# Optimization experiments

Measured on AMD Instinct MI355X. Metric: run time of the kernel, lower is better.

The kernel has to match this reference:

```python
import jax, jax.numpy as jnp
import numpy as np

D = 256       # d_model
NH = 8        # heads
K = 7         # neighborhood kernel size
DFF = 1024    # feedforward dim
EPS = 1e-5
B, H, W = 4, 56, 56


def layer_norm(x, g, b):
    m = jnp.mean(x, axis=-1, keepdims=True)
    v = jnp.mean((x - m) ** 2, axis=-1, keepdims=True)
    return (x - m) * jax.lax.rsqrt(v + EPS) * g + b


def neighborhood_attn(x, W_qkv, b_qkv, W_proj, b_proj):
    # NATTEN NeighborhoodAttention2D: each query attends to a KxK window
    # centered on it, clamped (shifted) at borders so every query sees K*K keys.
    Bx, Hx, Wx, C = x.shape
    hd = C // NH
    qkv = x @ W_qkv + b_qkv                      # [B,H,W,3C]
    q, k, v = jnp.split(qkv, 3, axis=-1)
    q = q.reshape(Bx, Hx, Wx, NH, hd)
    k = k.reshape(Bx, Hx, Wx, NH, hd)
    v = v.reshape(Bx, Hx, Wx, NH, hd)
    # neighbor index grids: start = clip(i - K//2, 0, H-K), window = start + [0..K)
    ih = jnp.clip(jnp.arange(Hx) - K // 2, 0, Hx - K)[:, None] + jnp.arange(K)  # [H,K]
    iw = jnp.clip(jnp.arange(Wx) - K // 2, 0, Wx - K)[:, None] + jnp.arange(K)  # [W,K]
    # gather K/V neighborhoods -> [B,H,W,K,K,NH,hd]
    k_nb = k[:, ih[:, None, :, None], iw[None, :, None, :]]
    v_nb = v[:, ih[:, None, :, None], iw[None, :, None, :]]
    attn = jnp.einsum('bhwnd,bhwijnd->bhwnij', q, k_nb) * (hd ** -0.5)
    attn = jax.nn.softmax(attn.reshape(Bx, Hx, Wx, NH, K * K), axis=-1)
    attn = attn.reshape(Bx, Hx, Wx, NH, K, K)
    out = jnp.einsum('bhwnij,bhwijnd->bhwnd', attn, v_nb).reshape(Bx, Hx, Wx, C)
    return out @ W_proj + b_proj


def setup_inputs() -> dict:
    key = jax.random.key(0)
    ks = jax.random.split(key, 8)
    s = 0.02
    return {
        'x': jax.random.normal(ks[0], (B, H, W, D), dtype=jnp.float32),
        'W_qkv': jax.random.normal(ks[1], (D, 3 * D), dtype=jnp.float32) * s,
        'b_qkv': jnp.zeros((3 * D,), dtype=jnp.float32),
        'W_proj': jax.random.normal(ks[2], (D, D), dtype=jnp.float32) * s,
        'b_proj': jnp.zeros((D,), dtype=jnp.float32),
        'W1': jax.random.normal(ks[3], (D, DFF), dtype=jnp.float32) * s,
        'b1': jnp.zeros((DFF,), dtype=jnp.float32),
        'W2': jax.random.normal(ks[4], (DFF, D), dtype=jnp.float32) * s,
        'b2': jnp.zeros((D,), dtype=jnp.float32),
        'g1': jnp.ones((D,), dtype=jnp.float32),
        'be1': jnp.zeros((D,), dtype=jnp.float32),
        'g2': jnp.ones((D,), dtype=jnp.float32),
        'be2': jnp.zeros((D,), dtype=jnp.float32),
    }


def reference(x, W_qkv, b_qkv, W_proj, b_proj, W1, b1, W2, b2, g1, be1, g2, be2):
    # norm_first=False (post-norm): x = norm1(x + mha(x)); x = norm2(x + ff(x))
    a = neighborhood_attn(x, W_qkv, b_qkv, W_proj, b_proj)
    x = layer_norm(x + a, g1, be1)
    f = jax.nn.relu(x @ W1 + b1) @ W2 + b2
    return layer_norm(x + f, g2, be2)
```

## Files before the change

kernel.cpp:

```cpp
#include <hip/hip_runtime.h>
#include <math.h>

#define BATCH 4
#define HH 56
#define WW 56
#define DMODEL 256
#define NHEADS 8
#define HD 32
#define NNB 49
#define NTOK (BATCH*HH*WW)

#define HALO 22
#define NHTOK (HALO*HALO)
#define KV_PAD 40

typedef __attribute__((ext_vector_type(8))) short s16x8;
typedef __attribute__((ext_vector_type(4))) float f32x4;
typedef __attribute__((ext_vector_type(2))) float f32x2;

__device__ inline unsigned short f2b(float f) {
    union { float f; unsigned int u; } v; v.f = f;
    unsigned int r = v.u + 0x7FFF + ((v.u >> 16) & 1);
    return (unsigned short)(r >> 16);
}
__device__ inline float b2f(unsigned short u) {
    union { float f; unsigned int u; } v; v.u = ((unsigned int)u) << 16;
    return v.f;
}

__device__ __forceinline__ f32x2 unpk(unsigned int u) {
    union { unsigned int u; float f; } lo, hi;
    lo.u = u << 16;
    hi.u = u & 0xffff0000u;
    return f32x2{lo.f, hi.f};
}

__device__ __forceinline__ f32x2 pk_fma(f32x2 a, f32x2 b, f32x2 c) {
#if __has_builtin(__builtin_elementwise_fma)
    return __builtin_elementwise_fma(a, b, c);
#else
    return f32x2{fmaf(a.x, b.x, c.x), fmaf(a.y, b.y, c.y)};
#endif
}

__device__ __forceinline__ void async16(const unsigned short* g, unsigned short* l) {
    __builtin_amdgcn_global_load_lds(
        (const __attribute__((address_space(1))) unsigned int*)g,
        (__attribute__((address_space(3))) unsigned int*)l, 16, 0, 0);
}

#define WAITV(N) { asm volatile("s_waitcnt vmcnt(" #N ")" ::: "memory"); }
#define BAR()    { __builtin_amdgcn_s_barrier(); __builtin_amdgcn_sched_barrier(0); }

#define XCAST_BLOCKS 1568

__device__ __forceinline__ void transpose_tile(
    const float* __restrict__ src, unsigned short* __restrict__ dst,
    int K, int N, int kt, int nt, int tid, float* lds )
{
    const int k0 = kt * 64, n0 = nt * 64;
    #pragma unroll
    for (int p = 0; p < 4; ++p) {
        const int r  = p * 16 + (tid >> 4);
        const int c4 = (tid & 15) * 4;
        const float4 v = *(const float4*)(src + (size_t)(k0 + r) * N + n0 + c4);
        lds[r * 65 + c4 + 0] = v.x; lds[r * 65 + c4 + 1] = v.y;
        lds[r * 65 + c4 + 2] = v.z; lds[r * 65 + c4 + 3] = v.w;
    }
    __syncthreads();
    #pragma unroll
    for (int p = 0; p < 4; ++p) {
        const int c  = p * 16 + (tid >> 4);
        const int k4 = (tid & 15) * 4;
        ushort4 o;
        o.x = f2b(lds[(k4 + 0) * 65 + c]);
        o.y = f2b(lds[(k4 + 1) * 65 + c]);
        o.z = f2b(lds[(k4 + 2) * 65 + c]);
        o.w = f2b(lds[(k4 + 3) * 65 + c]);
        *(ushort4*)(dst + (size_t)(n0 + c) * K + k0 + k4) = o;
    }
}

__global__ __launch_bounds__(256)
void prep_kernel(const float* __restrict__ x,
                 const float* __restrict__ Wq, const float* __restrict__ Wp,
                 const float* __restrict__ W1, const float* __restrict__ W2,
                 unsigned short* __restrict__ xb,
                 unsigned short* __restrict__ Wqb, unsigned short* __restrict__ Wpb,
                 unsigned short* __restrict__ W1b, unsigned short* __restrict__ W2b)
{
    __shared__ float lds[64 * 65];
    const int tid = threadIdx.x;
    if (blockIdx.x < XCAST_BLOCKS) {
        const int i = blockIdx.x * 256 + tid;
        const float4* xp = (const float4*)x + (size_t)i * 2;
        const float4 a = xp[0], b = xp[1];
        s16x8 o;
        o[0] = (short)f2b(a.x); o[1] = (short)f2b(a.y);
        o[2] = (short)f2b(a.z); o[3] = (short)f2b(a.w);
        o[4] = (short)f2b(b.x); o[5] = (short)f2b(b.y);
        o[6] = (short)f2b(b.z); o[7] = (short)f2b(b.w);
        *((s16x8*)xb + i) = o;
        return;
    }
    int wb = blockIdx.x - XCAST_BLOCKS;
    if (wb < 48) {
        transpose_tile(Wq, Wqb, 256, 768, wb & 3, wb >> 2, tid, lds);
    } else if ((wb -= 48) < 16) {
        transpose_tile(Wp, Wpb, 256, 256, wb & 3, wb >> 2, tid, lds);
    } else if ((wb -= 16) < 64) {
        transpose_tile(W1, W1b, 256, 1024, wb & 3, wb >> 2, tid, lds);
    } else {
        wb -= 64;
        transpose_tile(W2, W2b, 1024, 256, wb & 15, wb >> 4, tid, lds);
    }
}

__global__ __launch_bounds__(256)
void gemm_k(const unsigned short* __restrict__ Ab,
            const unsigned short* __restrict__ Bt, const float* __restrict__ bias,
            unsigned short* __restrict__ outb,
            int N, int K, int relu)
{
    __shared__ unsigned short As[2][128 * 64];
    __shared__ unsigned short Bs[2][128 * 64];

    const int tid = threadIdx.x;

    const int nwg = gridDim.x;
    const int q8 = nwg >> 3, r8 = nwg & 7;
    const int xcd = blockIdx.x & 7, pos = blockIdx.x >> 3;
    const int d = (xcd < r8 ? xcd * (q8 + 1) : r8 * (q8 + 1) + (xcd - r8) * q8) + pos;
    const int nbx = N >> 7;
    const int bm = (d / nbx) * 128, bn = (d % nbx) * 128;

    const int wid = tid >> 6, lane = tid & 63;
    const int wm = (wid >> 1) * 64, wn = (wid & 1) * 64;
    const int row16 = lane & 15, quad = lane >> 4;
    const int crow = lane >> 3;
    const int ckS = ((lane & 7) ^ crow) * 8;

    f32x4 acc[4][4] = {};

    auto stage = [&](int buf, int k0) {
        #pragma unroll
        for (int c = 0; c < 4; ++c) {
            const int ch = wid * 4 + c;
            async16(Ab + (size_t)(bm + ch * 8 + crow) * K + k0 + ckS, As[buf] + ch * 512);
        }
        #pragma unroll
        for (int c = 0; c < 4; ++c) {
            const int ch = wid * 4 + c;
            async16(Bt + (size_t)(bn + ch * 8 + crow) * K + k0 + ckS, Bs[buf] + ch * 512);
        }
    };
    auto compute = [&](int buf) {
        #pragma unroll
        for (int kc = 0; kc < 2; ++kc) {
            s16x8 af[4], bf[4];
            #pragma unroll
            for (int i = 0; i < 4; ++i)
                af[i] = *(const s16x8*)(As[buf] + (wm + i * 16 + row16) * 64
                                        + (((kc * 4 + quad) ^ (row16 & 7)) * 8));
            #pragma unroll
            for (int j = 0; j < 4; ++j)
                bf[j] = *(const s16x8*)(Bs[buf] + (wn + j * 16 + row16) * 64
                                        + (((kc * 4 + quad) ^ (row16 & 7)) * 8));
            #pragma unroll
            for (int i = 0; i < 4; ++i)
                #pragma unroll
                for (int j = 0; j < 4; ++j)
                    acc[i][j] = __builtin_amdgcn_mfma_f32_16x16x32_bf16(af[i], bf[j], acc[i][j], 0, 0, 0);
        }
    };

    stage(0, 0);
    stage(1, 64);
    const int nsteps = K >> 6;
    for (int s = 0; s < nsteps; ++s) {
        const int buf = s & 1;
        if (s == nsteps - 1) WAITV(0) else WAITV(8)
        BAR()
        compute(buf);
        BAR()
        if (s + 2 < nsteps) stage(buf, (s + 2) << 6);
    }

    unsigned short* Cs = (unsigned short*)As;
    #pragma unroll
    for (int j = 0; j < 4; ++j) {
        const int col = wn + j * 16 + row16;
        const float bb = bias[bn + col];
        #pragma unroll
        for (int i = 0; i < 4; ++i) {
            const int rr = wm + i * 16 + quad * 4;
            #pragma unroll
            for (int reg = 0; reg < 4; ++reg) {
                float v = acc[i][j][reg] + bb;
                if (relu) v = fmaxf(v, 0.f);
                Cs[(rr + reg) * 128 + col] = f2b(v);
            }
        }
    }
    __syncthreads();
    #pragma unroll
    for (int p = 0; p < 8; ++p) {
        const int s = p * 256 + tid;
        const int rr = s >> 4, cb = (s & 15) * 8;
        *(s16x8*)(outb + (size_t)(bm + rr) * N + bn + cb) = *(const s16x8*)(Cs + rr * 128 + cb);
    }
}

__global__ __launch_bounds__(512)
void gemm_ln(const unsigned short* __restrict__ Ab, const unsigned short* __restrict__ Bt,
             const float* __restrict__ bias, const float* __restrict__ resid,
             const float* __restrict__ g, const float* __restrict__ beta,
             float* __restrict__ outf, unsigned short* __restrict__ outb, int K)
{
    __shared__ unsigned short As[2][64 * 64];
    __shared__ unsigned short Bs[2][256 * 64];

    const int tid = threadIdx.x;
    const int bm = blockIdx.x * 64;
    const int wid = tid >> 6, lane = tid & 63;
    const int wm = (wid >> 2) * 32, wn = (wid & 3) * 64;
    const int wc = wid & 3;
    const int row16 = lane & 15, quad = lane >> 4;
    const int crow = lane >> 3;
    const int ckS = ((lane & 7) ^ crow) * 8;

    f32x4 acc[2][4] = {};

    auto stage = [&](int buf, int k0) {
        #pragma unroll
        for (int c = 0; c < 5; ++c) {
            const int ch = wid * 5 + c;
            if (ch < 8) {
                async16(Ab + (size_t)(bm + ch * 8 + crow) * K + k0 + ckS, As[buf] + ch * 512);
            } else {
                const int bc = ch - 8;
                async16(Bt + (size_t)(bc * 8 + crow) * K + k0 + ckS, Bs[buf] + bc * 512);
            }
        }
    };
    auto compute = [&](int buf) {
        #pragma unroll
        for (int kc = 0; kc < 2; ++kc) {
            s16x8 af[2], bf[4];
            #pragma unroll
            for (int i = 0; i < 2; ++i)
                af[i] = *(const s16x8*)(As[buf] + (wm + i * 16 + row16) * 64
                                        + (((kc * 4 + quad) ^ (row16 & 7)) * 8));
            #pragma unroll
            for (int j = 0; j < 4; ++j)
                bf[j] = *(const s16x8*)(Bs[buf] + (wn + j * 16 + row16) * 64
                                        + (((kc * 4 + quad) ^ (row16 & 7)) * 8));
            #pragma unroll
            for (int i = 0; i < 2; ++i)
                #pragma unroll
                for (int j = 0; j < 4; ++j)
                    acc[i][j] = __builtin_amdgcn_mfma_f32_16x16x32_bf16(af[i], bf[j], acc[i][j], 0, 0, 0);
        }
    };

    stage(0, 0);
    stage(1, 64);
    const int nsteps = K >> 6;
    for (int s = 0; s < nsteps; ++s) {
        const int buf = s & 1;
        if (s == nsteps - 1) WAITV(0) else WAITV(5)
        BAR()
        compute(buf);
        BAR()
        if (s + 2 < nsteps) stage(buf, (s + 2) << 6);
    }

    float bb[4], gv[4], bev[4];
    #pragma unroll
    for (int j = 0; j < 4; ++j) {
        const int col = wn + j * 16 + row16;
        bb[j] = bias[col]; gv[j] = g[col]; bev[j] = beta[col];
    }
    #pragma unroll
    for (int i = 0; i < 2; ++i) {
        #pragma unroll
        for (int reg = 0; reg < 4; ++reg) {
            const size_t rb = (size_t)(bm + wm + i * 16 + quad * 4 + reg) * 256;
            #pragma unroll
            for (int j = 0; j < 4; ++j)
                acc[i][j][reg] += bb[j] + resid[rb + wn + j * 16 + row16];
        }
    }

    float* red = (float*)As[0];
    #pragma unroll
    for (int i = 0; i < 2; ++i) {
        #pragma unroll
        for (int reg = 0; reg < 4; ++reg) {
            float s1 = 0.f, s2 = 0.f;
            #pragma unroll
            for (int j = 0; j < 4; ++j) {
                const float t = acc[i][j][reg];
                s1 += t; s2 += t * t;
            }
            #pragma unroll
            for (int o = 1; o < 16; o <<= 1) {
                s1 += __shfl_xor(s1, o, 64);
                s2 += __shfl_xor(s2, o, 64);
            }
            if (row16 == 0) {
                const int lrow = wm + i * 16 + quad * 4 + reg;
                red[lrow * 8 + wc * 2]     = s1;
                red[lrow * 8 + wc * 2 + 1] = s2;
            }
        }
    }
    __syncthreads();
    float* stats = red + 512;
    if (tid < 64) {
        const float S1 = red[tid*8] + red[tid*8+2] + red[tid*8+4] + red[tid*8+6];
        const float S2 = red[tid*8+1] + red[tid*8+3] + red[tid*8+5] + red[tid*8+7];
        const float m = S1 * (1.0f / 256.0f);
        const float var = S2 * (1.0f / 256.0f) - m * m;
        stats[tid * 2]     = m;
        stats[tid * 2 + 1] = rsqrtf(var + 1e-5f);
    }
    __syncthreads();

    #pragma unroll
    for (int i = 0; i < 2; ++i) {
        #pragma unroll
        for (int reg = 0; reg < 4; ++reg) {
            const int lrow = wm + i * 16 + quad * 4 + reg;
            const float m = stats[lrow * 2], r = stats[lrow * 2 + 1];
            const size_t rb = (size_t)(bm + lrow) * 256;
            #pragma unroll
            for (int j = 0; j < 4; ++j) {
                const int col = wn + j * 16 + row16;
                const float o = (acc[i][j][reg] - m) * r * gv[j] + bev[j];
                outf[rb + col] = o;
                if (outb) outb[rb + col] = f2b(o);
            }
        }
    }
}

__global__ __launch_bounds__(256, 2)
void natt_kernel(const unsigned short* __restrict__ qkvb, unsigned short* __restrict__ att)
{
    const int blk  = blockIdx.x;
    const int head = blk & 7;
    const int t2   = blk >> 3;
    const int tile = t2 & 15;
    const int b    = t2 >> 4;
    const int r0 = (tile >> 2) * 16, c0 = (tile & 3) * 16;
    const int hs = min(max(r0 - 3, 0), 34);
    const int ws = min(max(c0 - 3, 0), 34);

    __shared__ unsigned short Ks[NHTOK * KV_PAD];
    __shared__ unsigned short Vs[NHTOK * KV_PAD];

    const int tid = threadIdx.x;

    #pragma unroll
    for (int it = 0; it < 8; ++it) {
        const int t = it * 64 + (tid >> 2);
        if (t < NHTOK) {
            const int hr = t / HALO, hc = t - hr * HALO;
            const size_t rb = ((size_t)((b * 56 + hs + hr) * 56 + (ws + hc))) * 768;
            const int d8 = (tid & 3) * 8;
            *(s16x8*)(Ks + t * KV_PAD + d8) = *(const s16x8*)(qkvb + rb + 256 + head * 32 + d8);
            *(s16x8*)(Vs + t * KV_PAD + d8) = *(const s16x8*)(qkvb + rb + 512 + head * 32 + d8);
        }
    }

    const int qh = min(r0 + (tid >> 4), 55);
    const int qw = min(c0 + (tid & 15), 55);
    const int tok = (b * 56 + qh) * 56 + qw;
    const int ro = min(max(qh - 3, 0), 49) - hs;
    const int co = min(max(qw - 3, 0), 49) - ws;

    f32x2 qf[16];
    {
        const unsigned int* qp = (const unsigned int*)(qkvb + (size_t)tok * 768 + head * 32);
        #pragma unroll
        for (int p = 0; p < 16; ++p)
            qf[p] = unpk(qp[p]) * (0.17677669529663687f * 1.4426950408889634f);
    }
    __syncthreads();

    f32x2 acc[16] = {};
    float sum = 0.f;
    for (int i = 0; i < 7; ++i) {
        const int trow = (ro + i) * HALO + co;

        float s[7];
        #pragma unroll
        for (int j = 0; j < 7; ++j) {
            const unsigned int* kp = (const unsigned int*)(Ks + (trow + j) * KV_PAD);
            const uint4 ka = *(const uint4*)(kp);
            const uint4 kb = *(const uint4*)(kp + 4);
            const uint4 kc = *(const uint4*)(kp + 8);
            const uint4 kd = *(const uint4*)(kp + 12);
            f32x2 sa = {0.f, 0.f}, sb = {0.f, 0.f};
            sa = pk_fma(qf[0],  unpk(ka.x), sa);  sb = pk_fma(qf[1],  unpk(ka.y), sb);
            sa = pk_fma(qf[2],  unpk(ka.z), sa);  sb = pk_fma(qf[3],  unpk(ka.w), sb);
            sa = pk_fma(qf[4],  unpk(kb.x), sa);  sb = pk_fma(qf[5],  unpk(kb.y), sb);
            sa = pk_fma(qf[6],  unpk(kb.z), sa);  sb = pk_fma(qf[7],  unpk(kb.w), sb);
            sa = pk_fma(qf[8],  unpk(kc.x), sa);  sb = pk_fma(qf[9],  unpk(kc.y), sb);
            sa = pk_fma(qf[10], unpk(kc.z), sa);  sb = pk_fma(qf[11], unpk(kc.w), sb);
            sa = pk_fma(qf[12], unpk(kd.x), sa);  sb = pk_fma(qf[13], unpk(kd.y), sb);
            sa = pk_fma(qf[14], unpk(kd.z), sa);  sb = pk_fma(qf[15], unpk(kd.w), sb);
            s[j] = sa.x + sa.y + sb.x + sb.y;
        }

        float p[7];
        #pragma unroll
        for (int j = 0; j < 7; ++j) {
            asm("v_exp_f32 %0, %1" : "=v"(p[j]) : "v"(s[j]));
        }
        #pragma unroll
        for (int j = 0; j < 7; ++j) sum += p[j];

        #pragma unroll
        for (int j = 0; j < 7; ++j) {
            const unsigned int* vp = (const unsigned int*)(Vs + (trow + j) * KV_PAD);
            const uint4 va = *(const uint4*)(vp);
            const uint4 vb = *(const uint4*)(vp + 4);
            const uint4 vc = *(const uint4*)(vp + 8);
            const uint4 vd = *(const uint4*)(vp + 12);
            const f32x2 pv = {p[j], p[j]};
            acc[0]  = pk_fma(pv, unpk(va.x), acc[0]);
            acc[1]  = pk_fma(pv, unpk(va.y), acc[1]);
            acc[2]  = pk_fma(pv, unpk(va.z), acc[2]);
            acc[3]  = pk_fma(pv, unpk(va.w), acc[3]);
            acc[4]  = pk_fma(pv, unpk(vb.x), acc[4]);
            acc[5]  = pk_fma(pv, unpk(vb.y), acc[5]);
            acc[6]  = pk_fma(pv, unpk(vb.z), acc[6]);
            acc[7]  = pk_fma(pv, unpk(vb.w), acc[7]);
            acc[8]  = pk_fma(pv, unpk(vc.x), acc[8]);
            acc[9]  = pk_fma(pv, unpk(vc.y), acc[9]);
            acc[10] = pk_fma(pv, unpk(vc.z), acc[10]);
            acc[11] = pk_fma(pv, unpk(vc.w), acc[11]);
            acc[12] = pk_fma(pv, unpk(vd.x), acc[12]);
            acc[13] = pk_fma(pv, unpk(vd.y), acc[13]);
            acc[14] = pk_fma(pv, unpk(vd.z), acc[14]);
            acc[15] = pk_fma(pv, unpk(vd.w), acc[15]);
        }
    }
    const float inv = 1.0f / sum;

    unsigned short* op = att + (size_t)tok * DMODEL + head * 32;
    #pragma unroll
    for (int d4 = 0; d4 < 8; ++d4) {
        ushort4 o;
        o.x = f2b(acc[d4 * 2].x     * inv);
        o.y = f2b(acc[d4 * 2].y     * inv);
        o.z = f2b(acc[d4 * 2 + 1].x * inv);
        o.w = f2b(acc[d4 * 2 + 1].y * inv);
        *(ushort4*)(op + d4 * 4) = o;
    }
}

extern "C" void kernel_launch(void* const* d_in, const int* in_sizes, int n_in,
                              void* d_out, int out_size, void* d_ws, size_t ws_size,
                              hipStream_t stream)
{
    const float* x      = (const float*)d_in[0];
    const float* W_qkv  = (const float*)d_in[1];
    const float* b_qkv  = (const float*)d_in[2];
    const float* W_proj = (const float*)d_in[3];
    const float* b_proj = (const float*)d_in[4];
    const float* W1     = (const float*)d_in[5];
    const float* b1     = (const float*)d_in[6];
    const float* W2     = (const float*)d_in[7];
    const float* b2     = (const float*)d_in[8];
    const float* g1     = (const float*)d_in[9];
    const float* be1    = (const float*)d_in[10];
    const float* g2     = (const float*)d_in[11];
    const float* be2    = (const float*)d_in[12];
    float* out = (float*)d_out;

    char* ws = (char*)d_ws;
    const int M = NTOK;

    unsigned short* qkvb = (unsigned short*)ws;
    unsigned short* h    = (unsigned short*)ws;
    unsigned short* attb = (unsigned short*)(ws + 38535168);
    float*          xn   = (float*)(ws + 57802752);
    unsigned short* xnb  = (unsigned short*)(ws + 70647808);
    unsigned short* Wqb  = (unsigned short*)(ws + 77070336);
    unsigned short* Wpb  = Wqb + 196608;
    unsigned short* W1b  = Wpb + 65536;
    unsigned short* W2b  = W1b + 262144;
    unsigned short* xb   = (unsigned short*)(ws + 78643200);

    dim3 blk(256);

    prep_kernel<<<dim3(XCAST_BLOCKS + 48 + 16 + 64 + 64), blk, 0, stream>>>(
        x, W_qkv, W_proj, W1, W2, xb, Wqb, Wpb, W1b, W2b);

    gemm_k<<<dim3(6 * 98), blk, 0, stream>>>(xb, Wqb, b_qkv, qkvb, 768, 256, 0);

    natt_kernel<<<dim3(512), blk, 0, stream>>>(qkvb, attb);

    gemm_ln<<<dim3(M / 64), dim3(512), 0, stream>>>(attb, Wpb, b_proj, x, g1, be1, xn, xnb, 256);

    gemm_k<<<dim3(8 * 98), blk, 0, stream>>>(xnb, W1b, b1, h, 1024, 256, 1);

    gemm_ln<<<dim3(M / 64), dim3(512), 0, stream>>>(h, W2b, b2, xn, g2, be2, out, nullptr, 1024);
}
```

Measured before the change: 175.3 us.

## Rewrite neighborhood attention kernel to use bf16 MFMA for QK and PV

Replaces the per-thread scalar packed-FMA neighborhood attention with a wave-level formulation on MFMA 16x16x32 bf16 instructions. Each wave handles four query rows of 16 columns and loops over halo rows, computing scores against 32 keys, masking those outside the 7-wide window, and staging probabilities through LDS for the PV product. V is stored transposed in LDS and K uses a padded row layout. The aim is to move the dot products onto matrix units. The cost is wasted work on masked keys, probability rounding to bf16, extra LDS traffic and waits, and a more complex output path.

```diff
diff --git a/kernel.cpp b/kernel.cpp
--- a/kernel.cpp
+++ b/kernel.cpp
@@ -12,11 +12,9 @@
 
 #define HALO 22
 #define NHTOK (HALO*HALO)
-#define KV_PAD 40
 
 typedef __attribute__((ext_vector_type(8))) short s16x8;
 typedef __attribute__((ext_vector_type(4))) float f32x4;
-typedef __attribute__((ext_vector_type(2))) float f32x2;
 
 __device__ inline unsigned short f2b(float f) {
     union { float f; unsigned int u; } v; v.f = f;
@@ -26,21 +24,6 @@
 __device__ inline float b2f(unsigned short u) {
     union { float f; unsigned int u; } v; v.u = ((unsigned int)u) << 16;
     return v.f;
-}
-
-__device__ __forceinline__ f32x2 unpk(unsigned int u) {
-    union { unsigned int u; float f; } lo, hi;
-    lo.u = u << 16;
-    hi.u = u & 0xffff0000u;
-    return f32x2{lo.f, hi.f};
-}
-
-__device__ __forceinline__ f32x2 pk_fma(f32x2 a, f32x2 b, f32x2 c) {
-#if __has_builtin(__builtin_elementwise_fma)
-    return __builtin_elementwise_fma(a, b, c);
-#else
-    return f32x2{fmaf(a.x, b.x, c.x), fmaf(a.y, b.y, c.y)};
-#endif
 }
 
 __device__ __forceinline__ void async16(const unsigned short* g, unsigned short* l) {
@@ -357,108 +340,154 @@
     const int hs = min(max(r0 - 3, 0), 34);
     const int ws = min(max(c0 - 3, 0), 34);
 
-    __shared__ unsigned short Ks[NHTOK * KV_PAD];
-    __shared__ unsigned short Vs[NHTOK * KV_PAD];
+    __shared__ __attribute__((aligned(16))) unsigned short Ks[(22*24 + 8) * 32];
+    __shared__ __attribute__((aligned(16))) unsigned short Vt[22*32*24 + 64];
+    __shared__ __attribute__((aligned(16))) unsigned short Ps[4 * 2 * 16 * 32];
 
     const int tid = threadIdx.x;
+    const int wid = tid >> 6, lane = tid & 63;
+    const int l15 = lane & 15, quad = lane >> 4;
+    unsigned short* Psw = Ps + wid * 1024;
+
+    const s16x8 zz = {};
+    for (int t = tid; t < 44; t += 256) {
+        const int hr = t >> 1, hc = 22 + (t & 1);
+        #pragma unroll
+        for (int d8 = 0; d8 < 32; d8 += 8)
+            *(s16x8*)(Ks + (hr*24 + hc)*32 + d8) = zz;
+    }
+    if (tid < 32)
+        *(s16x8*)(Ks + (528 + (tid >> 2))*32 + (tid & 3)*8) = zz;
+    for (int t = tid; t < 704; t += 256)
+        *(unsigned int*)(Vt + t*24 + 22) = 0u;
+    if (tid < 8)
+        *(s16x8*)(Vt + 22*32*24 + tid*8) = zz;
 
     #pragma unroll
     for (int it = 0; it < 8; ++it) {
         const int t = it * 64 + (tid >> 2);
         if (t < NHTOK) {
             const int hr = t / HALO, hc = t - hr * HALO;
-            const size_t rb = ((size_t)((b * 56 + hs + hr) * 56 + (ws + hc))) * 768;
+            const size_t rb = ((size_t)((b*56 + hs + hr)*56 + (ws + hc))) * 768;
             const int d8 = (tid & 3) * 8;
-            *(s16x8*)(Ks + t * KV_PAD + d8) = *(const s16x8*)(qkvb + rb + 256 + head * 32 + d8);
-            *(s16x8*)(Vs + t * KV_PAD + d8) = *(const s16x8*)(qkvb + rb + 512 + head * 32 + d8);
-        }
-    }
-
-    const int qh = min(r0 + (tid >> 4), 55);
-    const int qw = min(c0 + (tid & 15), 55);
-    const int tok = (b * 56 + qh) * 56 + qw;
-    const int ro = min(max(qh - 3, 0), 49) - hs;
-    const int co = min(max(qw - 3, 0), 49) - ws;
-
-    f32x2 qf[16];
-    {
-        const unsigned int* qp = (const unsigned int*)(qkvb + (size_t)tok * 768 + head * 32);
-        #pragma unroll
-        for (int p = 0; p < 16; ++p)
-            qf[p] = unpk(qp[p]) * (0.17677669529663687f * 1.4426950408889634f);
-    }
+            *(s16x8*)(Ks + (hr*24 + hc)*32 + d8) =
+                *(const s16x8*)(qkvb + rb + 256 + head*32 + d8);
+        }
+    }
+    if (tid < 242) {
+        const int hr = tid / 11, ph = tid - hr * 11, hc = ph * 2;
+        const size_t rb0 = ((size_t)((b*56 + hs + hr)*56 + (ws + hc))) * 768 + 512 + head*32;
+        unsigned int wa[16], wb[16];
+        #pragma unroll
+        for (int k = 0; k < 4; ++k) {
+            *(uint4*)(wa + k*4) = *(const uint4*)((const unsigned int*)(qkvb + rb0) + k*4);
+            *(uint4*)(wb + k*4) = *(const uint4*)((const unsigned int*)(qkvb + rb0 + 768) + k*4);
+        }
+        #pragma unroll
+        for (int d = 0; d < 32; ++d) {
+            const unsigned int a  = (wa[d>>1] >> ((d&1)*16)) & 0xffffu;
+            const unsigned int bv = (wb[d>>1] >> ((d&1)*16)) & 0xffffu;
+            *(unsigned int*)(Vt + (hr*32 + d)*24 + hc) = a | (bv << 16);
+        }
+    }
+
+    s16x8 qf[4];
+    int rs[4];
+    #pragma unroll
+    for (int r = 0; r < 4; ++r) {
+        const int qh = min(r0 + wid*4 + r, 55);
+        rs[r] = min(max(qh - 3, 0), 49) - hs;
+        const int qw = min(c0 + l15, 55);
+        qf[r] = *(const s16x8*)(qkvb + (size_t)((b*56+qh)*56+qw)*768 + head*32 + quad*8);
+    }
+    const int qwl = min(c0 + l15, 55);
+    const int cs = min(max(qwl - 3, 0), 49) - ws;
     __syncthreads();
 
-    f32x2 acc[16] = {};
-    float sum = 0.f;
-    for (int i = 0; i < 7; ++i) {
-        const int trow = (ro + i) * HALO + co;
-
-        float s[7];
-        #pragma unroll
-        for (int j = 0; j < 7; ++j) {
-            const unsigned int* kp = (const unsigned int*)(Ks + (trow + j) * KV_PAD);
-            const uint4 ka = *(const uint4*)(kp);
-            const uint4 kb = *(const uint4*)(kp + 4);
-            const uint4 kc = *(const uint4*)(kp + 8);
-            const uint4 kd = *(const uint4*)(kp + 12);
-            f32x2 sa = {0.f, 0.f}, sb = {0.f, 0.f};
-            sa = pk_fma(qf[0],  unpk(ka.x), sa);  sb = pk_fma(qf[1],  unpk(ka.y), sb);
-            sa = pk_fma(qf[2],  unpk(ka.z), sa);  sb = pk_fma(qf[3],  unpk(ka.w), sb);
-            sa = pk_fma(qf[4],  unpk(kb.x), sa);  sb = pk_fma(qf[5],  unpk(kb.y), sb);
-            sa = pk_fma(qf[6],  unpk(kb.z), sa);  sb = pk_fma(qf[7],  unpk(kb.w), sb);
-            sa = pk_fma(qf[8],  unpk(kc.x), sa);  sb = pk_fma(qf[9],  unpk(kc.y), sb);
-            sa = pk_fma(qf[10], unpk(kc.z), sa);  sb = pk_fma(qf[11], unpk(kc.w), sb);
-            sa = pk_fma(qf[12], unpk(kd.x), sa);  sb = pk_fma(qf[13], unpk(kd.y), sb);
-            sa = pk_fma(qf[14], unpk(kd.z), sa);  sb = pk_fma(qf[15], unpk(kd.w), sb);
-            s[j] = sa.x + sa.y + sb.x + sb.y;
-        }
-
-        float p[7];
-        #pragma unroll
-        for (int j = 0; j < 7; ++j) {
-            asm("v_exp_f32 %0, %1" : "=v"(p[j]) : "v"(s[j]));
-        }
-        #pragma unroll
-        for (int j = 0; j < 7; ++j) sum += p[j];
-
-        #pragma unroll
-        for (int j = 0; j < 7; ++j) {
-            const unsigned int* vp = (const unsigned int*)(Vs + (trow + j) * KV_PAD);
-            const uint4 va = *(const uint4*)(vp);
-            const uint4 vb = *(const uint4*)(vp + 4);
-            const uint4 vc = *(const uint4*)(vp + 8);
-            const uint4 vd = *(const uint4*)(vp + 12);
-            const f32x2 pv = {p[j], p[j]};
-            acc[0]  = pk_fma(pv, unpk(va.x), acc[0]);
-            acc[1]  = pk_fma(pv, unpk(va.y), acc[1]);
-            acc[2]  = pk_fma(pv, unpk(va.z), acc[2]);
-            acc[3]  = pk_fma(pv, unpk(va.w), acc[3]);
-            acc[4]  = pk_fma(pv, unpk(vb.x), acc[4]);
-            acc[5]  = pk_fma(pv, unpk(vb.y), acc[5]);
-            acc[6]  = pk_fma(pv, unpk(vb.z), acc[6]);
-            acc[7]  = pk_fma(pv, unpk(vb.w), acc[7]);
-            acc[8]  = pk_fma(pv, unpk(vc.x), acc[8]);
-            acc[9]  = pk_fma(pv, unpk(vc.y), acc[9]);
-            acc[10] = pk_fma(pv, unpk(vc.z), acc[10]);
-            acc[11] = pk_fma(pv, unpk(vc.w), acc[11]);
-            acc[12] = pk_fma(pv, unpk(vd.x), acc[12]);
-            acc[13] = pk_fma(pv, unpk(vd.y), acc[13]);
-            acc[14] = pk_fma(pv, unpk(vd.z), acc[14]);
-            acc[15] = pk_fma(pv, unpk(vd.w), acc[15]);
-        }
-    }
-    const float inv = 1.0f / sum;
-
-    unsigned short* op = att + (size_t)tok * DMODEL + head * 32;
-    #pragma unroll
-    for (int d4 = 0; d4 < 8; ++d4) {
-        ushort4 o;
-        o.x = f2b(acc[d4 * 2].x     * inv);
-        o.y = f2b(acc[d4 * 2].y     * inv);
-        o.z = f2b(acc[d4 * 2 + 1].x * inv);
-        o.w = f2b(acc[d4 * 2 + 1].y * inv);
-        *(ushort4*)(op + d4 * 4) = o;
+    f32x4 out[4][2] = {};
+    float ssum[4] = {};
+    const float SCL = 0.17677669529663687f * 1.4426950408889634f;
+    const int rsmin = min(min(rs[0], rs[1]), min(rs[2], rs[3]));
+    const int rsmax = max(max(rs[0], rs[1]), max(rs[2], rs[3]));
+
+    auto qk_phase = [&](int r, int bufo, const s16x8& ka, const s16x8& kb) {
+        const f32x4 z = {0.f, 0.f, 0.f, 0.f};
+        f32x4 s0 = __builtin_amdgcn_mfma_f32_16x16x32_bf16(ka, qf[r], z, 0, 0, 0);
+        f32x4 s1 = __builtin_amdgcn_mfma_f32_16x16x32_bf16(kb, qf[r], z, 0, 0, 0);
+        float p0[4], p1[4];
+        #pragma unroll
+        for (int j = 0; j < 4; ++j) {
+            float e0, e1;
+            asm("v_exp_f32 %0, %1" : "=v"(e0) : "v"(s0[j] * SCL));
+            asm("v_exp_f32 %0, %1" : "=v"(e1) : "v"(s1[j] * SCL));
+            const int c0i = quad*4 + j;
+            p0[j] = ((unsigned)(c0i - cs)      < 7u) ? e0 : 0.f;
+            p1[j] = ((unsigned)(c0i + 16 - cs) < 7u) ? e1 : 0.f;
+            ssum[r] += p0[j] + p1[j];
+        }
+        unsigned int u00, u01, u10, u11;
+        asm("v_cvt_pk_bf16_f32 %0, %1, %2" : "=v"(u00) : "v"(p0[0]), "v"(p0[1]));
+        asm("v_cvt_pk_bf16_f32 %0, %1, %2" : "=v"(u01) : "v"(p0[2]), "v"(p0[3]));
+        asm("v_cvt_pk_bf16_f32 %0, %1, %2" : "=v"(u10) : "v"(p1[0]), "v"(p1[1]));
+        asm("v_cvt_pk_bf16_f32 %0, %1, %2" : "=v"(u11) : "v"(p1[2]), "v"(p1[3]));
+        uint2 w0; w0.x = u00; w0.y = u01;
+        uint2 w1; w1.x = u10; w1.y = u11;
+        *(uint2*)(Psw + bufo + l15*32 + quad*4)      = w0;
+        *(uint2*)(Psw + bufo + l15*32 + 16 + quad*4) = w1;
+    };
+    auto pv_phase = [&](int r, int bufo, const s16x8& v0, const s16x8& v1) {
+        s16x8 pf = *(const s16x8*)(Psw + bufo + l15*32 + quad*8);
+        out[r][0] = __builtin_amdgcn_mfma_f32_16x16x32_bf16(pf, v0, out[r][0], 0, 0, 0);
+        out[r][1] = __builtin_amdgcn_mfma_f32_16x16x32_bf16(pf, v1, out[r][1], 0, 0, 0);
+    };
+
+    for (int hi = rsmin; hi <= rsmax + 6; ++hi) {
+        const s16x8 ka = *(const s16x8*)(Ks + (hi*24 + l15)*32 + quad*8);
+        const s16x8 kb = *(const s16x8*)(Ks + (hi*24 + 16 + l15)*32 + quad*8);
+        const s16x8 v0 = *(const s16x8*)(Vt + (hi*32 + l15)*24 + quad*8);
+        const s16x8 v1 = *(const s16x8*)(Vt + (hi*32 + 16 + l15)*24 + quad*8);
+        #pragma unroll
+        for (int rp = 0; rp < 2; ++rp) {
+            const int ra = rp*2, rb_ = rp*2 + 1;
+            const bool Aa = (unsigned)(hi - rs[ra])  < 7u;
+            const bool Ab = (unsigned)(hi - rs[rb_]) < 7u;
+            if (Aa) qk_phase(ra, 0, ka, kb);
+            if (Ab) qk_phase(rb_, 512, ka, kb);
+            if (Aa || Ab) {
+                asm volatile("s_waitcnt lgkmcnt(0)" ::: "memory");
+                __builtin_amdgcn_sched_barrier(0);
+            }
+            if (Aa) pv_phase(ra, 0, v0, v1);
+            if (Ab) pv_phase(rb_, 512, v0, v1);
+        }
+    }
+
+    float invs[4];
+    #pragma unroll
+    for (int r = 0; r < 4; ++r) {
+        float s = ssum[r];
+        s += __shfl_xor(s, 16, 64);
+        s += __shfl_xor(s, 32, 64);
+        invs[r] = 1.0f / s;
+    }
+    unsigned short* Csw = Psw;
+    #pragma unroll
+    for (int r = 0; r < 4; ++r) {
+        asm volatile("s_waitcnt lgkmcnt(0)" ::: "memory");
+        __builtin_amdgcn_sched_barrier(0);
+        #pragma unroll
+        for (int reg = 0; reg < 4; ++reg) {
+            const float iv = __shfl(invs[r], quad*4 + reg, 64);
+            Csw[(quad*4+reg)*32 + l15]      = f2b(out[r][0][reg] * iv);
+            Csw[(quad*4+reg)*32 + 16 + l15] = f2b(out[r][1][reg] * iv);
+        }
+        asm volatile("s_waitcnt lgkmcnt(0)" ::: "memory");
+        __builtin_amdgcn_sched_barrier(0);
+        const int qc = lane >> 2, ch = lane & 3;
+        const int qh = min(r0 + wid*4 + r, 55);
+        const int qw = min(c0 + qc, 55);
+        *(s16x8*)(att + (size_t)((b*56+qh)*56+qw)*256 + head*32 + ch*8) =
+            *(const s16x8*)(Csw + qc*32 + ch*8);
     }
 }
 
```

Result: faster. 164.9 us, median of 2 (-5.9%).
